# Optimization experiments

Hardware: AMD Instinct MI355X
Metric: run time of the kernel (lower is better)

The kernel has to match this reference:

```python
import jax, jax.numpy as jnp
import numpy as np

B, N, K, H, D = 2, 8192, 16, 4, 32
C_IN, C_OUT = 64, 128
HD = H * D


def setup_inputs() -> dict:
    key = jax.random.key(0)
    ks = jax.random.split(key, 16)
    s = 0.02
    return {
        "xyzs": jax.random.normal(ks[0], (B, N, 3), jnp.float32),
        "features": jax.random.normal(ks[1], (B, N, C_IN), jnp.float32),
        "k_graph": jax.random.randint(ks[2], (B, N, K), 0, N),
        # projections (stored as [in, out]; torch Linear applies x @ W.T)
        "Wk": jax.random.normal(ks[3], (C_IN, HD), jnp.float32) * s,
        "Wv": jax.random.normal(ks[4], (C_IN, HD), jnp.float32) * s,
        "Wq": jax.random.normal(ks[5], (C_IN, HD), jnp.float32) * s,
        # aggregate MLP: Linear(HD,HD) -> ReLU -> Linear(HD,H)
        "A1": jax.random.normal(ks[6], (HD, HD), jnp.float32) * s,
        "b1": jnp.zeros((HD,), jnp.float32),
        "A2": jax.random.normal(ks[7], (HD, H), jnp.float32) * s,
        "b2": jnp.zeros((H,), jnp.float32),
        # position MLP: Linear(3,3) -> ReLU -> Linear(3,HD)
        "P1": jax.random.normal(ks[8], (3, 3), jnp.float32) * s,
        "bp1": jnp.zeros((3,), jnp.float32),
        "P2": jax.random.normal(ks[9], (3, HD), jnp.float32) * s,
        "bp2": jnp.zeros((HD,), jnp.float32),
        # output projection Linear(HD, C_OUT)
        "Wout": jax.random.normal(ks[10], (HD, C_OUT), jnp.float32) * s,
        "bout": jnp.zeros((C_OUT,), jnp.float32),
    }


def reference(xyzs, features, k_graph, Wk, Wv, Wq, A1, b1, A2, b2,
              P1, bp1, P2, bp2, Wout, bout):
    # KNN gather (irregular access): [B,N,K,*]
    nbr_feat = jax.vmap(lambda f, g: f[g])(features, k_graph)   # [B,N,K,C_IN]
    nbr_xyz = jax.vmap(lambda x, g: x[g])(xyzs, k_graph)        # [B,N,K,3]

    rel_pos = xyzs[:, :, None, :] - nbr_xyz                      # [B,N,K,3]
    pe = jax.nn.relu(rel_pos @ P1 + bp1) @ P2 + bp2              # [B,N,K,HD]

    keys = nbr_feat @ Wk                                         # [B,N,K,HD]
    values = nbr_feat @ Wv                                       # [B,N,K,HD]
    queries = features @ Wq                                      # [B,N,HD]

    # subtraction attention + aggregate MLP -> per-head logits
    attn = queries[:, :, None, :] - keys + pe                    # [B,N,K,HD]
    attn = jax.nn.relu(attn @ A1 + b1) @ A2 + b2                 # [B,N,K,H]
    attn = jax.nn.softmax(attn, axis=-2)                         # softmax over K

    # weighted reduce over neighbors
    fv = (values + pe).reshape(B, N, K, H, D)
    fused = jnp.sum(attn[..., None] * fv, axis=2)                # [B,N,H,D]
    fused = fused.reshape(B, N, HD)
    return fused @ Wout + bout                                   # [B,N,C_OUT]
```

## Files before the change

kernel.cpp:

```cpp
#include <hip/hip_runtime.h>
#include <hip/hip_bf16.h>

#define BATCH 2
#define NPTS  8192
#define BN    (BATCH * NPTS)
#define KNN   16
#define HEADS 4
#define HD    128
#define CIN   64
#define COUT  128
#define WCOLS 384

using short8  = __attribute__((ext_vector_type(8))) short;
using float4v = __attribute__((ext_vector_type(4))) float;

static __device__ __forceinline__ unsigned short f2bf(float x) {
    unsigned u = __float_as_uint(x);
    u += 0x7fffu + ((u >> 16) & 1u);
    return (unsigned short)(u >> 16);
}
static __device__ __forceinline__ float bf_lo(unsigned u) { return __uint_as_float(u << 16); }
static __device__ __forceinline__ float bf_hi(unsigned u) { return __uint_as_float(u & 0xffff0000u); }
static __device__ __forceinline__ unsigned pack2(float a, float b) {
    return (unsigned)f2bf(a) | ((unsigned)f2bf(b) << 16);
}
static __device__ __forceinline__ void unpack8(uint4 u, float* f) {
    f[0] = bf_lo(u.x); f[1] = bf_hi(u.x);
    f[2] = bf_lo(u.y); f[3] = bf_hi(u.y);
    f[4] = bf_lo(u.z); f[5] = bf_hi(u.z);
    f[6] = bf_lo(u.w); f[7] = bf_hi(u.w);
}

template <int CTRL>
static __device__ __forceinline__ float dpp_mov(float x) {
    return __int_as_float(
        __builtin_amdgcn_update_dpp(0, __float_as_int(x), CTRL, 0xf, 0xf, false));
}
static __device__ __forceinline__ float ror_sum16(float x) {
    x += dpp_mov<0x128>(x);
    x += dpp_mov<0x124>(x);
    x += dpp_mov<0x122>(x);
    x += dpp_mov<0x121>(x);
    return x;
}
static __device__ __forceinline__ float ror_max16(float x) {
    x = fmaxf(x, dpp_mov<0x128>(x));
    x = fmaxf(x, dpp_mov<0x124>(x));
    x = fmaxf(x, dpp_mov<0x122>(x));
    x = fmaxf(x, dpp_mov<0x121>(x));
    return x;
}

__global__ void prep_kernel(const float* __restrict__ Wk,
                            const float* __restrict__ Wv,
                            const float* __restrict__ Wq,
                            const float* __restrict__ A1,
                            const float* __restrict__ b1,
                            const float* __restrict__ P2,
                            const float* __restrict__ bp2,
                            const float* __restrict__ Wout,
                            unsigned short* __restrict__ WcatT,
                            unsigned short* __restrict__ WoutT,
                            float* __restrict__ P2A1,
                            float* __restrict__ cvec) {
    int t = blockIdx.x * blockDim.x + threadIdx.x;
    if (t < WCOLS * CIN) {
        int n = t >> 6, kk = t & 63;
        float val;
        if (n < 2 * HD) {
            const float* w = (n < HD ? Wq : Wk) + kk * HD;
            int jj = n & (HD - 1);
            float acc = 0.f;
            #pragma unroll 4
            for (int m = 0; m < HD; m += 4) {
                float4 wr = *(const float4*)(w + m);
                acc += wr.x * A1[(m+0)*HD + jj] + wr.y * A1[(m+1)*HD + jj]
                     + wr.z * A1[(m+2)*HD + jj] + wr.w * A1[(m+3)*HD + jj];
            }
            val = acc;
        } else {
            val = Wv[kk * HD + (n - 2 * HD)];
        }
        WcatT[t] = f2bf(val);
    } else if (t < WCOLS * CIN + COUT * HD) {
        int u = t - WCOLS * CIN;
        int n = u >> 7, kk = u & 127;
        WoutT[u] = f2bf(Wout[kk * COUT + n]);
    } else if (t < WCOLS * CIN + COUT * HD + 3 * HD) {
        int u = t - (WCOLS * CIN + COUT * HD);
        int r = u / HD, j = u % HD;
        const float* w = P2 + r * HD;
        float acc = 0.f;
        #pragma unroll 4
        for (int m = 0; m < HD; m += 4) {
            float4 wr = *(const float4*)(w + m);
            acc += wr.x * A1[(m+0)*HD + j] + wr.y * A1[(m+1)*HD + j]
                 + wr.z * A1[(m+2)*HD + j] + wr.w * A1[(m+3)*HD + j];
        }
        P2A1[u] = acc;
    } else if (t < WCOLS * CIN + COUT * HD + 3 * HD + HD) {
        int j = t - (WCOLS * CIN + COUT * HD + 3 * HD);
        float acc = b1[j];
        #pragma unroll 4
        for (int m = 0; m < HD; m += 4) {
            float4 wr = *(const float4*)(bp2 + m);
            acc += wr.x * A1[(m+0)*HD + j] + wr.y * A1[(m+1)*HD + j]
                 + wr.z * A1[(m+2)*HD + j] + wr.w * A1[(m+3)*HD + j];
        }
        cvec[j] = acc;
    }
}

#define AK 88
__global__ __launch_bounds__(256) void qkv_kernel(const float* __restrict__ F,
                                                  const unsigned short* __restrict__ WcatT,
                                                  const float* __restrict__ cvec,
                                                  unsigned short* __restrict__ QKVb) {
    __shared__ unsigned short Af[64 * AK];
    __shared__ unsigned short Bf[WCOLS * AK];
    int p0 = blockIdx.x * 64;
    int t = threadIdx.x;

    #pragma unroll
    for (int i = 0; i < 4; ++i) {
        int v = t + i * 256;
        int row = v >> 4, c4 = (v & 15) * 4;
        float4 fa = *(const float4*)(F + (p0 + row) * CIN + c4);
        uint2 u = make_uint2(pack2(fa.x, fa.y), pack2(fa.z, fa.w));
        *(uint2*)(&Af[row * AK + c4]) = u;
    }
    #pragma unroll
    for (int i = 0; i < 12; ++i) {
        int v = t + i * 256;
        int n = v >> 3, j16 = v & 7;
        *(uint4*)(&Bf[n * AK + j16 * 8]) = ((const uint4*)WcatT)[v];
    }
    __syncthreads();

    int w = t >> 6, l = t & 63;
    int ml = l & 15, quad = l >> 4;
    int m0 = w * 16;

    short8 a0 = *(const short8*)(&Af[(m0 + ml) * AK + quad * 8]);
    short8 a1 = *(const short8*)(&Af[(m0 + ml) * AK + 32 + quad * 8]);

    #pragma unroll
    for (int nt = 0; nt < 24; ++nt) {
        short8 b0 = *(const short8*)(&Bf[(nt * 16 + ml) * AK + quad * 8]);
        short8 b1 = *(const short8*)(&Bf[(nt * 16 + ml) * AK + 32 + quad * 8]);
        float4v acc = {0.f, 0.f, 0.f, 0.f};
        acc = __builtin_amdgcn_mfma_f32_16x16x32_bf16(a0, b0, acc, 0, 0, 0);
        acc = __builtin_amdgcn_mfma_f32_16x16x32_bf16(a1, b1, acc, 0, 0, 0);
        int n = nt * 16 + ml;
        float cadd = (n < HD) ? cvec[n] : 0.f;
        #pragma unroll
        for (int r = 0; r < 4; ++r) {
            int row = p0 + m0 + quad * 4 + r;
            QKVb[row * WCOLS + n] = f2bf(acc[r] + cadd);
        }
    }
}

__global__ __launch_bounds__(256) void attn_kernel(
        const float* __restrict__ xyzs, const int* __restrict__ kg,
        const unsigned short* __restrict__ QKVb,
        const float* __restrict__ P1, const float* __restrict__ bp1,
        const float* __restrict__ P2, const float* __restrict__ bp2,
        const float* __restrict__ P2A1,
        const float* __restrict__ A2, const float* __restrict__ b2,
        unsigned short* __restrict__ FUSEDb) {
    __shared__ float4 A2s[HD];
    __shared__ float4 WAs[HD];
    __shared__ float4 P2s[HD];
    int t = threadIdx.x;
    if (t < HD) {
        A2s[t] = *(const float4*)(A2 + t * 4);
        WAs[t] = make_float4(P2A1[t], P2A1[HD + t], P2A1[2 * HD + t], 0.f);
        P2s[t] = make_float4(P2[t], P2[HD + t], P2[2 * HD + t], bp2[t]);
    }
    __syncthreads();

    int lane = t & 63;
    int p = blockIdx.x * 4 + (t >> 6);
    int b = p >> 13;
    int k = lane & 15, cg = lane >> 4;
    int c0 = cg * 32;

    int idx = kg[p * KNN + k];
    int q = b * NPTS + idx;

    float r0 = xyzs[p * 3 + 0] - xyzs[q * 3 + 0];
    float r1 = xyzs[p * 3 + 1] - xyzs[q * 3 + 1];
    float r2 = xyzs[p * 3 + 2] - xyzs[q * 3 + 2];
    float h0 = fmaxf(r0 * P1[0] + r1 * P1[3] + r2 * P1[6] + bp1[0], 0.f);
    float h1 = fmaxf(r0 * P1[1] + r1 * P1[4] + r2 * P1[7] + bp1[1], 0.f);
    float h2 = fmaxf(r0 * P1[2] + r1 * P1[5] + r2 * P1[8] + bp1[2], 0.f);

    const uint4* qp = (const uint4*)(QKVb + (size_t)p * WCOLS + c0);
    const uint4* kp = (const uint4*)(QKVb + (size_t)q * WCOLS + HD + c0);
    const uint4* vp = (const uint4*)(QKVb + (size_t)q * WCOLS + 2 * HD + c0);
    uint4 quA[4] = {qp[0], qp[1], qp[2], qp[3]};
    uint4 kuA[4] = {kp[0], kp[1], kp[2], kp[3]};
    uint4 vuA[4] = {vp[0], vp[1], vp[2], vp[3]};

    float pl0 = 0.f, pl1 = 0.f, pl2 = 0.f, pl3 = 0.f;
    #pragma unroll
    for (int jc = 0; jc < 4; ++jc) {
        float qz[8], kr[8];
        unpack8(quA[jc], qz);
        unpack8(kuA[jc], kr);
        #pragma unroll
        for (int jj = 0; jj < 8; ++jj) {
            int ch = c0 + jc * 8 + jj;
            float4 wa = WAs[ch];
            float z = fmaxf(qz[jj] - kr[jj] + h0 * wa.x + h1 * wa.y + h2 * wa.z, 0.f);
            float4 ar = A2s[ch];
            pl0 += z * ar.x; pl1 += z * ar.y; pl2 += z * ar.z; pl3 += z * ar.w;
        }
    }
    pl0 += __shfl_xor(pl0, 16, 64); pl0 += __shfl_xor(pl0, 32, 64);
    pl1 += __shfl_xor(pl1, 16, 64); pl1 += __shfl_xor(pl1, 32, 64);
    pl2 += __shfl_xor(pl2, 16, 64); pl2 += __shfl_xor(pl2, 32, 64);
    pl3 += __shfl_xor(pl3, 16, 64); pl3 += __shfl_xor(pl3, 32, 64);

    float lgt = pl0;
    lgt = (cg == 1) ? pl1 : lgt;
    lgt = (cg == 2) ? pl2 : lgt;
    lgt = (cg == 3) ? pl3 : lgt;

    float m = ror_max16(lgt);
    float e = __expf(lgt - m);
    float s = ror_sum16(e);
    float a = e / s;

    float hb0 = ror_sum16(a * h0);
    float hb1 = ror_sum16(a * h1);
    float hb2 = ror_sum16(a * h2);

    #pragma unroll
    for (int jc = 0; jc < 4; ++jc) {
        float vr[8];
        unpack8(vuA[jc], vr);
        float wv[8];
        #pragma unroll
        for (int jj = 0; jj < 8; ++jj) wv[jj] = ror_sum16(a * vr[jj]);
        if (k == jc) {
            float f[8];
            #pragma unroll
            for (int jj = 0; jj < 8; ++jj) {
                float4 pp = P2s[c0 + jc * 8 + jj];
                f[jj] = wv[jj] + hb0 * pp.x + hb1 * pp.y + hb2 * pp.z + pp.w;
            }
            uint4 fu;
            fu.x = pack2(f[0], f[1]); fu.y = pack2(f[2], f[3]);
            fu.z = pack2(f[4], f[5]); fu.w = pack2(f[6], f[7]);
            *(uint4*)(FUSEDb + (size_t)p * HD + c0 + jc * 8) = fu;
        }
    }
}

#define OK2 144
__global__ __launch_bounds__(256) void out_kernel(const unsigned short* __restrict__ FUSEDb,
                                                  const unsigned short* __restrict__ WoutT,
                                                  const float* __restrict__ bout,
                                                  float* __restrict__ out) {
    __shared__ unsigned short Af[64 * OK2];
    __shared__ unsigned short Bf[HD * OK2];
    int p0 = blockIdx.x * 64;
    int t = threadIdx.x;

    #pragma unroll
    for (int i = 0; i < 4; ++i) {
        int v = t + i * 256;
        int row = v >> 4, j16 = v & 15;
        *(uint4*)(&Af[row * OK2 + j16 * 8]) = ((const uint4*)FUSEDb)[(p0 + row) * 16 + j16];
    }
    #pragma unroll
    for (int i = 0; i < 8; ++i) {
        int v = t + i * 256;
        int n = v >> 4, j16 = v & 15;
        *(uint4*)(&Bf[n * OK2 + j16 * 8]) = ((const uint4*)WoutT)[v];
    }
    __syncthreads();

    int w = t >> 6, l = t & 63;
    int ml = l & 15, quad = l >> 4;
    int m0 = w * 16;

    short8 af[4];
    #pragma unroll
    for (int ks = 0; ks < 4; ++ks)
        af[ks] = *(const short8*)(&Af[(m0 + ml) * OK2 + ks * 32 + quad * 8]);

    #pragma unroll
    for (int nt = 0; nt < 8; ++nt) {
        float4v acc = {0.f, 0.f, 0.f, 0.f};
        #pragma unroll
        for (int ks = 0; ks < 4; ++ks) {
            short8 bf = *(const short8*)(&Bf[(nt * 16 + ml) * OK2 + ks * 32 + quad * 8]);
            acc = __builtin_amdgcn_mfma_f32_16x16x32_bf16(af[ks], bf, acc, 0, 0, 0);
        }
        int n = nt * 16 + ml;
        float bo = bout[n];
        #pragma unroll
        for (int r = 0; r < 4; ++r) {
            int row = p0 + m0 + quad * 4 + r;
            out[row * COUT + n] = acc[r] + bo;
        }
    }
}

extern "C" void kernel_launch(void* const* d_in, const int* in_sizes, int n_in,
                              void* d_out, int out_size, void* d_ws, size_t ws_size,
                              hipStream_t stream) {
    const float* xyzs = (const float*)d_in[0];
    const float* feat = (const float*)d_in[1];
    const int*   kg   = (const int*)  d_in[2];
    const float* Wk   = (const float*)d_in[3];
    const float* Wv   = (const float*)d_in[4];
    const float* Wq   = (const float*)d_in[5];
    const float* A1   = (const float*)d_in[6];
    const float* b1   = (const float*)d_in[7];
    const float* A2   = (const float*)d_in[8];
    const float* b2   = (const float*)d_in[9];
    const float* P1   = (const float*)d_in[10];
    const float* bp1  = (const float*)d_in[11];
    const float* P2   = (const float*)d_in[12];
    const float* bp2  = (const float*)d_in[13];
    const float* Wout = (const float*)d_in[14];
    const float* bout = (const float*)d_in[15];
    float* out = (float*)d_out;

    float* ws = (float*)d_ws;
    float* cvec = ws;
    float* P2A1 = ws + 128;
    unsigned short* QKVb  = (unsigned short*)(ws + 512);
    unsigned short* FUSEDb = QKVb + (size_t)BN * WCOLS;
    unsigned short* WcatT = FUSEDb + (size_t)BN * HD;
    unsigned short* WoutT = WcatT + WCOLS * CIN;

    int prep_elems = WCOLS*CIN + COUT*HD + 3*HD + HD;
    prep_kernel<<<(prep_elems + 255) / 256, 256, 0, stream>>>(
        Wk, Wv, Wq, A1, b1, P2, bp2, Wout, WcatT, WoutT, P2A1, cvec);

    qkv_kernel<<<BN / 64, 256, 0, stream>>>(feat, WcatT, cvec, QKVb);

    attn_kernel<<<BN / 4, 256, 0, stream>>>(
        xyzs, kg, QKVb, P1, bp1, P2, bp2, P2A1, A2, b2, FUSEDb);

    out_kernel<<<BN / 64, 256, 0, stream>>>(FUSEDb, WoutT, bout, out);
}
```

Measured before the change: 140.2 us.

## Use packed fp32 math and a recursive-halving reduction in attention kernel

```diff
diff --git a/kernel.cpp b/kernel.cpp
--- a/kernel.cpp
+++ b/kernel.cpp
@@ -13,6 +13,7 @@
 
 using short8  = __attribute__((ext_vector_type(8))) short;
 using float4v = __attribute__((ext_vector_type(4))) float;
+using float2v = __attribute__((ext_vector_type(2))) float;
 
 static __device__ __forceinline__ unsigned short f2bf(float x) {
     unsigned u = __float_as_uint(x);
@@ -24,11 +25,38 @@
 static __device__ __forceinline__ unsigned pack2(float a, float b) {
     return (unsigned)f2bf(a) | ((unsigned)f2bf(b) << 16);
 }
-static __device__ __forceinline__ void unpack8(uint4 u, float* f) {
-    f[0] = bf_lo(u.x); f[1] = bf_hi(u.x);
-    f[2] = bf_lo(u.y); f[3] = bf_hi(u.y);
-    f[4] = bf_lo(u.z); f[5] = bf_hi(u.z);
-    f[6] = bf_lo(u.w); f[7] = bf_hi(u.w);
+static __device__ __forceinline__ float2v bf2pair(unsigned u) {
+    float2v r;
+    r.x = __uint_as_float(u << 16);
+    r.y = __uint_as_float(u & 0xffff0000u);
+    return r;
+}
+
+static __device__ __forceinline__ float2v pk_add(float2v a, float2v b) {
+    float2v d;
+    asm("v_pk_add_f32 %0, %1, %2" : "=v"(d) : "v"(a), "v"(b));
+    return d;
+}
+static __device__ __forceinline__ float2v pk_sub(float2v a, float2v b) {
+    float2v d;
+    asm("v_pk_add_f32 %0, %1, %2 neg_lo:[0,1] neg_hi:[0,1]" : "=v"(d) : "v"(a), "v"(b));
+    return d;
+}
+static __device__ __forceinline__ float2v pk_mul(float2v a, float2v b) {
+    float2v d;
+    asm("v_pk_mul_f32 %0, %1, %2" : "=v"(d) : "v"(a), "v"(b));
+    return d;
+}
+static __device__ __forceinline__ float2v pk_fma(float2v a, float2v b, float2v c) {
+    float2v d;
+    asm("v_pk_fma_f32 %0, %1, %2, %3" : "=v"(d) : "v"(a), "v"(b), "v"(c));
+    return d;
+}
+static __device__ __forceinline__ float2v sx2(float2v v, int mask) {
+    float2v r;
+    r.x = __shfl_xor(v.x, mask, 64);
+    r.y = __shfl_xor(v.y, mask, 64);
+    return r;
 }
 
 template <int CTRL>
@@ -169,15 +197,22 @@
         const float* __restrict__ P2A1,
         const float* __restrict__ A2, const float* __restrict__ b2,
         unsigned short* __restrict__ FUSEDb) {
-    __shared__ float4 A2s[HD];
-    __shared__ float4 WAs[HD];
+    __shared__ float4 A2pA[64];
+    __shared__ float4 A2pB[64];
+    __shared__ float4 WApA[64];
+    __shared__ float2 WApB[64];
     __shared__ float4 P2s[HD];
     int t = threadIdx.x;
-    if (t < HD) {
-        A2s[t] = *(const float4*)(A2 + t * 4);
-        WAs[t] = make_float4(P2A1[t], P2A1[HD + t], P2A1[2 * HD + t], 0.f);
-        P2s[t] = make_float4(P2[t], P2[HD + t], P2[2 * HD + t], bp2[t]);
-    }
+    if (t < 64) {
+        int c = t * 2;
+        float4 a2l = *(const float4*)(A2 + c * 4);
+        float4 a2h = *(const float4*)(A2 + (c + 1) * 4);
+        A2pA[t] = make_float4(a2l.x, a2h.x, a2l.y, a2h.y);
+        A2pB[t] = make_float4(a2l.z, a2h.z, a2l.w, a2h.w);
+        WApA[t] = make_float4(P2A1[c], P2A1[c + 1], P2A1[HD + c], P2A1[HD + c + 1]);
+        WApB[t] = make_float2(P2A1[2 * HD + c], P2A1[2 * HD + c + 1]);
+    }
+    if (t < HD) P2s[t] = make_float4(P2[t], P2[HD + t], P2[2 * HD + t], bp2[t]);
     __syncthreads();
 
     int lane = t & 63;
@@ -203,33 +238,52 @@
     uint4 kuA[4] = {kp[0], kp[1], kp[2], kp[3]};
     uint4 vuA[4] = {vp[0], vp[1], vp[2], vp[3]};
 
-    float pl0 = 0.f, pl1 = 0.f, pl2 = 0.f, pl3 = 0.f;
+    float2v h0p = {h0, h0}, h1p = {h1, h1}, h2p = {h2, h2};
+    float2v pl0 = {0.f, 0.f}, pl1 = {0.f, 0.f}, pl2 = {0.f, 0.f}, pl3 = {0.f, 0.f};
+    int pbase = cg * 16;
+
     #pragma unroll
     for (int jc = 0; jc < 4; ++jc) {
-        float qz[8], kr[8];
-        unpack8(quA[jc], qz);
-        unpack8(kuA[jc], kr);
-        #pragma unroll
-        for (int jj = 0; jj < 8; ++jj) {
-            int ch = c0 + jc * 8 + jj;
-            float4 wa = WAs[ch];
-            float z = fmaxf(qz[jj] - kr[jj] + h0 * wa.x + h1 * wa.y + h2 * wa.z, 0.f);
-            float4 ar = A2s[ch];
-            pl0 += z * ar.x; pl1 += z * ar.y; pl2 += z * ar.z; pl3 += z * ar.w;
-        }
-    }
-    pl0 += __shfl_xor(pl0, 16, 64); pl0 += __shfl_xor(pl0, 32, 64);
-    pl1 += __shfl_xor(pl1, 16, 64); pl1 += __shfl_xor(pl1, 32, 64);
-    pl2 += __shfl_xor(pl2, 16, 64); pl2 += __shfl_xor(pl2, 32, 64);
-    pl3 += __shfl_xor(pl3, 16, 64); pl3 += __shfl_xor(pl3, 32, 64);
-
-    float lgt = pl0;
-    lgt = (cg == 1) ? pl1 : lgt;
-    lgt = (cg == 2) ? pl2 : lgt;
-    lgt = (cg == 3) ? pl3 : lgt;
-
-    float m = ror_max16(lgt);
-    float e = __expf(lgt - m);
+        const unsigned* uq = (const unsigned*)&quA[jc];
+        const unsigned* uk = (const unsigned*)&kuA[jc];
+        #pragma unroll
+        for (int jp = 0; jp < 4; ++jp) {
+            float2v qp2 = bf2pair(uq[jp]);
+            float2v kp2 = bf2pair(uk[jp]);
+            int pi = pbase + jc * 4 + jp;
+            float4 wa = WApA[pi];
+            float2 wb = WApB[pi];
+            float2v acc = pk_sub(qp2, kp2);
+            acc = pk_fma(h0p, (float2v){wa.x, wa.y}, acc);
+            acc = pk_fma(h1p, (float2v){wa.z, wa.w}, acc);
+            acc = pk_fma(h2p, (float2v){wb.x, wb.y}, acc);
+            float2v z2;
+            z2.x = fmaxf(acc.x, 0.f);
+            z2.y = fmaxf(acc.y, 0.f);
+            float4 aA = A2pA[pi], aB = A2pB[pi];
+            pl0 = pk_fma(z2, (float2v){aA.x, aA.y}, pl0);
+            pl1 = pk_fma(z2, (float2v){aA.z, aA.w}, pl1);
+            pl2 = pk_fma(z2, (float2v){aB.x, aB.y}, pl2);
+            pl3 = pk_fma(z2, (float2v){aB.z, aB.w}, pl3);
+        }
+    }
+    float l0 = pl0.x + pl0.y;
+    float l1 = pl1.x + pl1.y;
+    float l2 = pl2.x + pl2.y;
+    float l3 = pl3.x + pl3.y;
+
+    l0 += __shfl_xor(l0, 16, 64); l0 += __shfl_xor(l0, 32, 64);
+    l1 += __shfl_xor(l1, 16, 64); l1 += __shfl_xor(l1, 32, 64);
+    l2 += __shfl_xor(l2, 16, 64); l2 += __shfl_xor(l2, 32, 64);
+    l3 += __shfl_xor(l3, 16, 64); l3 += __shfl_xor(l3, 32, 64);
+
+    float lgt = l0;
+    lgt = (cg == 1) ? l1 : lgt;
+    lgt = (cg == 2) ? l2 : lgt;
+    lgt = (cg == 3) ? l3 : lgt;
+
+    float m16 = ror_max16(lgt);
+    float e = __expf(lgt - m16);
     float s = ror_sum16(e);
     float a = e / s;
 
@@ -237,25 +291,59 @@
     float hb1 = ror_sum16(a * h1);
     float hb2 = ror_sum16(a * h2);
 
-    #pragma unroll
-    for (int jc = 0; jc < 4; ++jc) {
-        float vr[8];
-        unpack8(vuA[jc], vr);
-        float wv[8];
-        #pragma unroll
-        for (int jj = 0; jj < 8; ++jj) wv[jj] = ror_sum16(a * vr[jj]);
-        if (k == jc) {
-            float f[8];
-            #pragma unroll
-            for (int jj = 0; jj < 8; ++jj) {
-                float4 pp = P2s[c0 + jc * 8 + jj];
-                f[jj] = wv[jj] + hb0 * pp.x + hb1 * pp.y + hb2 * pp.z + pp.w;
-            }
-            uint4 fu;
-            fu.x = pack2(f[0], f[1]); fu.y = pack2(f[2], f[3]);
-            fu.z = pack2(f[4], f[5]); fu.w = pack2(f[6], f[7]);
-            *(uint4*)(FUSEDb + (size_t)p * HD + c0 + jc * 8) = fu;
-        }
+    float2v ap = {a, a};
+    float2v y0[4], y1[4], y2[4], y3[4];
+    {
+        const unsigned* v0 = (const unsigned*)&vuA[0];
+        const unsigned* v1 = (const unsigned*)&vuA[1];
+        const unsigned* v2 = (const unsigned*)&vuA[2];
+        const unsigned* v3 = (const unsigned*)&vuA[3];
+        #pragma unroll
+        for (int i = 0; i < 4; ++i) {
+            y0[i] = pk_mul(ap, bf2pair(v0[i]));
+            y1[i] = pk_mul(ap, bf2pair(v1[i]));
+            y2[i] = pk_mul(ap, bf2pair(v2[i]));
+            y3[i] = pk_mul(ap, bf2pair(v3[i]));
+        }
+    }
+    bool hi3 = (k & 8) != 0;
+    float2v k0[4], k1[4];
+    #pragma unroll
+    for (int i = 0; i < 4; ++i) {
+        float2v s0 = hi3 ? y0[i] : y2[i];
+        float2v s1 = hi3 ? y1[i] : y3[i];
+        float2v r0v = sx2(s0, 8);
+        float2v r1v = sx2(s1, 8);
+        k0[i] = pk_add(hi3 ? y2[i] : y0[i], r0v);
+        k1[i] = pk_add(hi3 ? y3[i] : y1[i], r1v);
+    }
+    bool hi2 = (k & 4) != 0;
+    float2v m2[4];
+    #pragma unroll
+    for (int i = 0; i < 4; ++i) {
+        float2v sv = hi2 ? k0[i] : k1[i];
+        float2v rv = sx2(sv, 4);
+        m2[i] = pk_add(hi2 ? k1[i] : k0[i], rv);
+    }
+    #pragma unroll
+    for (int i = 0; i < 4; ++i) m2[i] = pk_add(m2[i], sx2(m2[i], 2));
+    #pragma unroll
+    for (int i = 0; i < 4; ++i) m2[i] = pk_add(m2[i], sx2(m2[i], 1));
+
+    if ((k & 3) == 0) {
+        int jc = k >> 2;
+        float f[8];
+        #pragma unroll
+        for (int i = 0; i < 4; ++i) {
+            float4 pp0 = P2s[c0 + jc * 8 + 2 * i];
+            float4 pp1 = P2s[c0 + jc * 8 + 2 * i + 1];
+            f[2 * i]     = m2[i].x + hb0 * pp0.x + hb1 * pp0.y + hb2 * pp0.z + pp0.w;
+            f[2 * i + 1] = m2[i].y + hb0 * pp1.x + hb1 * pp1.y + hb2 * pp1.z + pp1.w;
+        }
+        uint4 fu;
+        fu.x = pack2(f[0], f[1]); fu.y = pack2(f[2], f[3]);
+        fu.z = pack2(f[4], f[5]); fu.w = pack2(f[6], f[7]);
+        *(uint4*)(FUSEDb + (size_t)p * HD + c0 + jc * 8) = fu;
     }
 }
 
```

After: 133.9 us (median of 2 runs). 4.5% less time.
